# Kernel tuning notes

Hardware: AMD Instinct MI355X
Metric: run time of the kernel (lower is better)

## Reference

```python
import jax, jax.numpy as jnp
import numpy as np

B, S, H, NH = 4, 2048, 768, 12
HD = H // NH

def _ln(x, g, b, eps=1e-5):
    m = jnp.mean(x, -1, keepdims=True)
    v = jnp.mean((x - m) ** 2, -1, keepdims=True)
    return (x - m) * jax.lax.rsqrt(v + eps) * g + b

def setup_inputs() -> dict:
    key = jax.random.key(0)
    ks = jax.random.split(key, 16)
    s = 0.02
    return {
        "x": jax.random.normal(ks[0], (B, S, H), jnp.float32),
        "prev_state": jax.random.normal(ks[1], (B, S, H), jnp.float32),
        "mask": jax.random.randint(ks[2], (B,), 0, 2).astype(bool),
        # depthwise conv1d (groups=H, k=3): torch weight [H, 1, 3] == OIH
        "conv_dw_w": jax.random.normal(ks[3], (H, 1, 3), jnp.float32) * s,
        "conv_dw_b": jnp.zeros((H,), jnp.float32),
        # pointwise conv1d (k=1) stored as [out, in]
        "conv_pw_w": jax.random.normal(ks[4], (H, H), jnp.float32) * s,
        "conv_pw_b": jnp.zeros((H,), jnp.float32),
        "cn_g": jnp.ones((H,), jnp.float32), "cn_b": jnp.zeros((H,), jnp.float32),
        "Wq": jax.random.normal(ks[5], (H, H), jnp.float32) * s, "bq": jnp.zeros((H,), jnp.float32),
        "Wk": jax.random.normal(ks[6], (H, H), jnp.float32) * s, "bk": jnp.zeros((H,), jnp.float32),
        "Wv": jax.random.normal(ks[7], (H, H), jnp.float32) * s, "bv": jnp.zeros((H,), jnp.float32),
        "Wo": jax.random.normal(ks[8], (H, H), jnp.float32) * s, "bo": jnp.zeros((H,), jnp.float32),
        "pn_g": jnp.ones((H,), jnp.float32), "pn_b": jnp.zeros((H,), jnp.float32),
        "Wpost": jax.random.normal(ks[9], (H, H), jnp.float32) * s, "bpost": jnp.zeros((H,), jnp.float32),
        "Wg": jax.random.normal(ks[10], (1, 2 * H), jnp.float32) * s, "bg": jnp.zeros((1,), jnp.float32),
    }

def reference(x, prev_state, mask, conv_dw_w, conv_dw_b, conv_pw_w, conv_pw_b,
              cn_g, cn_b, Wq, bq, Wk, bk, Wv, bv, Wo, bo,
              pn_g, pn_b, Wpost, bpost, Wg, bg):
    # ---- bridge: depthwise conv (k=3) -> pointwise conv (k=1) -> GELU -> LN ----
    mem_t = prev_state.transpose(0, 2, 1)  # [B, H, S]
    dw = jax.lax.conv_general_dilated(
        mem_t, conv_dw_w, window_strides=(1,), padding=[(1, 1)],
        feature_group_count=H, dimension_numbers=("NCH", "OIH", "NCH")) + conv_dw_b[None, :, None]
    pw = jnp.einsum("bhs,oh->bos", dw, conv_pw_w) + conv_pw_b[None, :, None]
    bridged = jax.nn.gelu(pw, approximate=False).transpose(0, 2, 1)  # [B, S, H]
    bridged = _ln(bridged, cn_g, cn_b)
    # ---- cross attention: q from x, k/v from bridged memory (nope, non-causal) ----
    q = (jnp.einsum("bsh,oh->bso", x, Wq) + bq).reshape(B, S, NH, HD)
    k = (jnp.einsum("bsh,oh->bso", bridged, Wk) + bk).reshape(B, S, NH, HD)
    v = (jnp.einsum("bsh,oh->bso", bridged, Wv) + bv).reshape(B, S, NH, HD)
    scores = jnp.einsum("bqnd,bknd->bnqk", q, k) / np.float32(np.sqrt(HD))
    attn = jax.nn.softmax(scores, axis=-1)
    ao = jnp.einsum("bnqk,bknd->bqnd", attn, v).reshape(B, S, H)
    ao = jnp.einsum("bsh,oh->bso", ao, Wo) + bo
    # ---- post-attn norm, linear, gate, scatter-add back under mask ----
    inj = _ln(ao, pn_g, pn_b)
    inj = jnp.einsum("bsh,oh->bso", inj, Wpost) + bpost
    gate = jax.nn.sigmoid(jnp.einsum("bsh,oh->bso", jnp.concatenate([x, bridged], -1), Wg) + bg)
    gated = gate * jnp.tanh(inj)
    mf = mask.astype(x.dtype)[:, None, None]  # batch-row select == masked scatter-add
    out = x + mf * gated
    # masked MSE aux loss (only over selected rows, as in the original)
    denom = jnp.maximum(mask.sum(), 1).astype(x.dtype) * np.float32(S * H)
    aux = jnp.sum(mf * (bridged - x) ** 2) / denom
    return out, aux
```

## Files before the change

kernel.cpp:

```cpp
#include <hip/hip_runtime.h>
#include <math.h>

#define B_ 4
#define S_ 2048
#define H_ 768
#define NH_ 12
#define HD_ 64
#define BSH (B_ * S_ * H_)
#define NROWS (B_ * S_)
#define WSZ (H_ * H_)

typedef __attribute__((ext_vector_type(8))) short bf16x8;
typedef __attribute__((ext_vector_type(4))) short s16x4;
typedef __attribute__((ext_vector_type(4))) float f32x4;
typedef __attribute__((ext_vector_type(2))) unsigned u32x2;
typedef __attribute__((ext_vector_type(4))) unsigned u32x4;

__device__ __forceinline__ short f2bf(float f) {
  union { float f; unsigned u; } x; x.f = f;
  unsigned r = x.u + 0x7FFF + ((x.u >> 16) & 1);
  return (short)(r >> 16);
}
__device__ __forceinline__ float bf2f(short s) {
  union { unsigned u; float f; } x;
  x.u = ((unsigned)(unsigned short)s) << 16;
  return x.f;
}
__device__ __forceinline__ unsigned bfpack(float lo, float hi) {
  union { float f; unsigned u; } a, b; a.f = lo; b.f = hi;
  return __builtin_amdgcn_perm(b.u, a.u, 0x07060302);
}

__device__ __forceinline__ float fexp2(float x) {
#if __has_builtin(__builtin_amdgcn_exp2f)
  return __builtin_amdgcn_exp2f(x);
#else
  float r;
  asm("v_exp_f32 %0, %1" : "=v"(r) : "v"(x));
  return r;
#endif
}

__device__ __forceinline__ void plswap32(unsigned& a, unsigned& b) {
#if __has_builtin(__builtin_amdgcn_permlane32_swap)
  u32x2 r = __builtin_amdgcn_permlane32_swap(a, b, false, false);
  a = r.x; b = r.y;
#else
  asm volatile("v_permlane32_swap_b32 %0, %1" : "+v"(a), "+v"(b));
#endif
}
__device__ __forceinline__ void plswap16(unsigned& a, unsigned& b) {
#if __has_builtin(__builtin_amdgcn_permlane16_swap)
  u32x2 r = __builtin_amdgcn_permlane16_swap(a, b, false, false);
  a = r.x; b = r.y;
#else
  asm volatile("v_permlane16_swap_b32 %0, %1" : "+v"(a), "+v"(b));
#endif
}

typedef __attribute__((address_space(1))) const unsigned int g_u32;
typedef __attribute__((address_space(3))) unsigned int l_u32;
__device__ __forceinline__ void gload16(const void* g, void* l) {
  __builtin_amdgcn_global_load_lds((g_u32*)g, (l_u32*)l, 16, 0, 0);
}

__global__ __launch_bounds__(256) void cvt_x_k(const float* __restrict__ src,
                                               short* __restrict__ dst) {
  int i = (blockIdx.x * 256 + threadIdx.x) * 4;
  float4 v = *(const float4*)(src + i);
  s16x4 o = {f2bf(v.x), f2bf(v.y), f2bf(v.z), f2bf(v.w)};
  *(s16x4*)(dst + i) = o;
}

__global__ __launch_bounds__(256) void cvt6_k(const float* w0, const float* w1,
                                              const float* w2, const float* w3,
                                              const float* w4, const float* w5,
                                              short* __restrict__ dst) {
  int i = (blockIdx.x * 256 + threadIdx.x) * 4;
  int m = i / WSZ;
  int off = i - m * WSZ;
  const float* s = m == 0 ? w0 : m == 1 ? w1 : m == 2 ? w2 : m == 3 ? w3 : m == 4 ? w4 : w5;
  float sc = (m == 1) ? 0.1803368802f : 1.0f;
  float4 v = *(const float4*)(s + off);
  s16x4 o = {f2bf(v.x * sc), f2bf(v.y * sc), f2bf(v.z * sc), f2bf(v.w * sc)};
  *(s16x4*)(dst + i) = o;
}

__global__ __launch_bounds__(192) void dwconv_k(const float* __restrict__ prev,
                                                const float* __restrict__ w3,
                                                const float* __restrict__ bias,
                                                short* __restrict__ out) {
  int row = blockIdx.x;
  int s = row & (S_ - 1);
  int h = threadIdx.x * 4;
  size_t base = (size_t)row * H_ + h;
  float4 c = *(const float4*)(prev + base);
  float4 wa = *(const float4*)(w3 + h * 3);
  float4 wb = *(const float4*)(w3 + h * 3 + 4);
  float4 wc = *(const float4*)(w3 + h * 3 + 8);
  float4 bi = *(const float4*)(bias + h);
  float4 acc;
  acc.x = bi.x + c.x * wa.y;
  acc.y = bi.y + c.y * wb.x;
  acc.z = bi.z + c.z * wb.w;
  acc.w = bi.w + c.w * wc.z;
  if (s > 0) {
    float4 l = *(const float4*)(prev + base - H_);
    acc.x += l.x * wa.x; acc.y += l.y * wa.w; acc.z += l.z * wb.z; acc.w += l.w * wc.y;
  }
  if (s < S_ - 1) {
    float4 r = *(const float4*)(prev + base + H_);
    acc.x += r.x * wa.z; acc.y += r.y * wb.y; acc.z += r.z * wc.x; acc.w += r.w * wc.w;
  }
  s16x4 o = {f2bf(acc.x), f2bf(acc.y), f2bf(acc.z), f2bf(acc.w)};
  *(s16x4*)(out + base) = o;
}

struct GemmJob {
  const short* A; const short* W; const float* bias; short* C; int act; int tout;
  float bscale;
};

__global__ __launch_bounds__(256) void gemm_bf2(GemmJob j0, GemmJob j1, GemmJob j2) {
  int d = blockIdx.x;
  int z = d / 384, r5 = d - z * 384;
  GemmJob j = z == 0 ? j0 : (z == 1 ? j1 : j2);
  int xcd = r5 & 7, s5 = r5 >> 3;
  int nx = s5 % 6, ny = xcd + 8 * (s5 / 6);
  __shared__ short As[128 * 64];
  __shared__ short Ws[128 * 64];
  int tid = threadIdx.x, lane = tid & 63, w = tid >> 6;
  int wr = w >> 1, wc = w & 1, lm = lane & 15, lq = lane >> 4;
  int m0 = ny * 128, n0 = nx * 128;
  int srow = lane >> 3;
  int skc = (lane & 7) * 8;
  const short* gA = j.A + (size_t)(m0 + w * 32 + srow) * H_ + skc;
  const short* gW = j.W + (size_t)(n0 + w * 32 + srow) * H_ + skc;
  short* lA = As + w * 2048;
  short* lW = Ws + w * 2048;

  f32x4 acc[4][4];
#pragma unroll
  for (int i = 0; i < 4; ++i)
#pragma unroll
    for (int jj = 0; jj < 4; ++jj) acc[i][jj] = (f32x4){0.f, 0.f, 0.f, 0.f};

  for (int kt = 0; kt < H_; kt += 64) {
    __syncthreads();
#pragma unroll
    for (int c = 0; c < 4; ++c) {
      gload16(gA + kt + (size_t)(c * 8) * H_, lA + c * 512);
      gload16(gW + kt + (size_t)(c * 8) * H_, lW + c * 512);
    }
    __syncthreads();
#pragma unroll
    for (int kk = 0; kk < 2; ++kk) {
      bf16x8 af[4], wf[4];
#pragma unroll
      for (int i = 0; i < 4; ++i)
        af[i] = *(const bf16x8*)&As[(wr * 64 + i * 16 + lm) * 64 + kk * 32 + lq * 8];
#pragma unroll
      for (int jj = 0; jj < 4; ++jj)
        wf[jj] = *(const bf16x8*)&Ws[(wc * 64 + jj * 16 + lm) * 64 + kk * 32 + lq * 8];
#pragma unroll
      for (int i = 0; i < 4; ++i)
#pragma unroll
        for (int jj = 0; jj < 4; ++jj)
          acc[i][jj] = __builtin_amdgcn_mfma_f32_16x16x32_bf16(af[i], wf[jj], acc[i][jj], 0, 0, 0);
    }
  }

  if (!j.tout) {
#pragma unroll
    for (int jj = 0; jj < 4; ++jj) {
      int col = n0 + wc * 64 + jj * 16 + lm;
      float bn = j.bias[col] * j.bscale;
#pragma unroll
      for (int i = 0; i < 4; ++i) {
        int mrow = m0 + wr * 64 + i * 16 + lq * 4;
#pragma unroll
        for (int r = 0; r < 4; ++r) {
          float cv = acc[i][jj][r] + bn;
          if (j.act) cv = 0.5f * cv * (1.0f + erff(cv * 0.70710678118f));
          j.C[(size_t)(mrow + r) * H_ + col] = f2bf(cv);
        }
      }
    }
  } else {
    int b = m0 >> 11;
    int sb = (m0 & (S_ - 1)) + wr * 64;
#pragma unroll
    for (int jj = 0; jj < 4; ++jj) {
      int col = n0 + wc * 64 + jj * 16 + lm;
      float bn = j.bias[col] * j.bscale;
      short* cp = j.C + ((size_t)(b * H_ + col)) * S_;
#pragma unroll
      for (int i = 0; i < 4; ++i) {
        int s = sb + i * 16 + lq * 4;
        s16x4 pk = {f2bf(acc[i][jj][0] + bn), f2bf(acc[i][jj][1] + bn),
                    f2bf(acc[i][jj][2] + bn), f2bf(acc[i][jj][3] + bn)};
        *(s16x4*)(cp + s) = pk;
      }
    }
  }
}

__global__ __launch_bounds__(256) void gemm_n64(const short* __restrict__ A,
                                                const short* __restrict__ W,
                                                const float* __restrict__ bias,
                                                short* __restrict__ C, int act) {
  int d = blockIdx.x;
  int xcd = d & 7, s5 = d >> 3;
  int nx = s5 % 12, ny = xcd + 8 * (s5 / 12);
  __shared__ short As[128 * 64];
  __shared__ short Ws[64 * 64];
  int tid = threadIdx.x, lane = tid & 63, w = tid >> 6;
  int wm = w >> 1, wn = w & 1, lm = lane & 15, lq = lane >> 4;
  int m0 = ny * 128, n0 = nx * 64;
  const short* gA = A + (size_t)(m0 + w * 32 + (lane >> 3)) * H_ + (lane & 7) * 8;
  const short* gW = W + (size_t)(n0 + w * 16 + (lane >> 3)) * H_ + (lane & 7) * 8;
  short* lA = As + w * 2048;
  short* lW = Ws + w * 1024;

  f32x4 acc[4][2];
#pragma unroll
  for (int i = 0; i < 4; ++i)
#pragma unroll
    for (int jj = 0; jj < 2; ++jj) acc[i][jj] = (f32x4){0.f, 0.f, 0.f, 0.f};

  for (int kt = 0; kt < H_; kt += 64) {
    __syncthreads();
#pragma unroll
    for (int c = 0; c < 4; ++c)
      gload16(gA + kt + (size_t)(c * 8) * H_, lA + c * 512);
#pragma unroll
    for (int c = 0; c < 2; ++c)
      gload16(gW + kt + (size_t)(c * 8) * H_, lW + c * 512);
    __syncthreads();
#pragma unroll
    for (int kk = 0; kk < 2; ++kk) {
      bf16x8 af[4], wf[2];
#pragma unroll
      for (int i = 0; i < 4; ++i)
        af[i] = *(const bf16x8*)&As[(wm * 64 + i * 16 + lm) * 64 + kk * 32 + lq * 8];
#pragma unroll
      for (int jj = 0; jj < 2; ++jj)
        wf[jj] = *(const bf16x8*)&Ws[(wn * 32 + jj * 16 + lm) * 64 + kk * 32 + lq * 8];
#pragma unroll
      for (int i = 0; i < 4; ++i)
#pragma unroll
        for (int jj = 0; jj < 2; ++jj)
          acc[i][jj] = __builtin_amdgcn_mfma_f32_16x16x32_bf16(af[i], wf[jj], acc[i][jj], 0, 0, 0);
    }
  }

#pragma unroll
  for (int jj = 0; jj < 2; ++jj) {
    int col = n0 + wn * 32 + jj * 16 + lm;
    float bn = bias[col];
#pragma unroll
    for (int i = 0; i < 4; ++i) {
      int mrow = m0 + wm * 64 + i * 16 + lq * 4;
#pragma unroll
      for (int r = 0; r < 4; ++r) {
        float cv = acc[i][jj][r] + bn;
        if (act) cv = 0.5f * cv * (1.0f + erff(cv * 0.70710678118f));
        C[(size_t)(mrow + r) * H_ + col] = f2bf(cv);
      }
    }
  }
}

__global__ __launch_bounds__(256) void ln_bf(const short* __restrict__ X,
                                             short* __restrict__ Y,
                                             const float* __restrict__ g,
                                             const float* __restrict__ bb) {
  int row = blockIdx.x;
  size_t base = (size_t)row * H_;
  int h0 = threadIdx.x, h1 = h0 + 256, h2 = h0 + 512;
  float x0 = bf2f(X[base + h0]), x1 = bf2f(X[base + h1]), x2 = bf2f(X[base + h2]);
  float s = x0 + x1 + x2;
  float s2 = x0 * x0 + x1 * x1 + x2 * x2;
  for (int off = 32; off > 0; off >>= 1) {
    s += __shfl_down(s, off);
    s2 += __shfl_down(s2, off);
  }
  __shared__ float sa[4], sq[4], st[2];
  int wid = threadIdx.x >> 6, lane = threadIdx.x & 63;
  if (lane == 0) { sa[wid] = s; sq[wid] = s2; }
  __syncthreads();
  if (threadIdx.x == 0) {
    float ts = sa[0] + sa[1] + sa[2] + sa[3];
    float ts2 = sq[0] + sq[1] + sq[2] + sq[3];
    float mean = ts * (1.0f / H_);
    float var = ts2 * (1.0f / H_) - mean * mean;
    st[0] = mean;
    st[1] = rsqrtf(var + 1e-5f);
  }
  __syncthreads();
  float mean = st[0], rstd = st[1];
  Y[base + h0] = f2bf((x0 - mean) * rstd * g[h0] + bb[h0]);
  Y[base + h1] = f2bf((x1 - mean) * rstd * g[h1] + bb[h1]);
  Y[base + h2] = f2bf((x2 - mean) * rstd * g[h2] + bb[h2]);
}

__global__ __launch_bounds__(256) void attn8_k(const short* __restrict__ qb,
                                               const short* __restrict__ kb,
                                               const short* __restrict__ vtb,
                                               short* __restrict__ aob) {
  __shared__ short Ks[2][64 * 64];
  __shared__ short Vt[2][64 * 64];
  int tid = threadIdx.x, lane = tid & 63, w = tid >> 6;
  int lm = lane & 15, lq = lane >> 4;
  int lm7 = lm & 7;
  int dd = blockIdx.x;
  int xcd = dd & 7, slot = dd >> 3;
  int g = xcd + 8 * (slot >> 4);
  int qx = slot & 15;
  int b = g / NH_, n = g - b * NH_;
  int q0 = qx * 128;
  int hoff = n * HD_;

  int rb8 = (lq ^ lm7) << 3;
  int rb8x = rb8 ^ 32;

  bf16x8 qf[2][2];
#pragma unroll
  for (int qg = 0; qg < 2; ++qg) {
    const short* qrow = qb + ((size_t)(b * S_ + q0 + w * 32 + qg * 16 + lm)) * H_ + hoff;
    qf[qg][0] = *(const bf16x8*)(qrow + lq * 8);
    qf[qg][1] = *(const bf16x8*)(qrow + 32 + lq * 8);
  }

  bf16x8 onef = {0x3F80, 0x3F80, 0x3F80, 0x3F80, 0x3F80, 0x3F80, 0x3F80, 0x3F80};
  f32x4 ls[2];
  ls[0] = (f32x4){0.f, 0.f, 0.f, 0.f};
  ls[1] = (f32x4){0.f, 0.f, 0.f, 0.f};

  f32x4 o[4][2];
#pragma unroll
  for (int i = 0; i < 4; ++i)
#pragma unroll
    for (int qg = 0; qg < 2; ++qg) o[i][qg] = (f32x4){0.f, 0.f, 0.f, 0.f};

  int jl = ((lane & 7) ^ (lane >> 3)) * 8;
  int rr = w * 16 + (lane >> 3);
  const short* kgl = kb + ((size_t)(b * S_ + rr)) * H_ + hoff + jl;
  const short* vgl = vtb + ((size_t)(b * H_ + hoff + rr)) * S_ + jl;
  int lbase = w * 1024;

#pragma unroll
  for (int c = 0; c < 2; ++c) {
    gload16(kgl + (size_t)(c * 8) * H_, &Ks[0][lbase + c * 512]);
    gload16(vgl + (size_t)(c * 8) * S_, &Vt[0][lbase + c * 512]);
  }

  for (int kt = 0, pb = 0; kt < S_; kt += 64, pb ^= 1) {
    __syncthreads();
    if (kt + 64 < S_) {
#pragma unroll
      for (int c = 0; c < 2; ++c) {
        gload16(kgl + (size_t)(kt + 64 + c * 8) * H_, &Ks[pb ^ 1][lbase + c * 512]);
        gload16(vgl + (size_t)(c * 8) * S_ + (kt + 64), &Vt[pb ^ 1][lbase + c * 512]);
      }
    }
    const short* Kw = &Ks[pb][0];
    const short* Vw = &Vt[pb][0];

    f32x4 st[4][2];
    __builtin_amdgcn_s_setprio(1);
#pragma unroll
    for (int ni = 0; ni < 4; ++ni) {
      int krow = (ni * 16 + lm) * 64;
      bf16x8 ka0 = *(const bf16x8*)&Kw[krow + rb8];
      bf16x8 ka1 = *(const bf16x8*)&Kw[krow + rb8x];
#pragma unroll
      for (int qg = 0; qg < 2; ++qg) {
        f32x4 z = (f32x4){0.f, 0.f, 0.f, 0.f};
        z = __builtin_amdgcn_mfma_f32_16x16x32_bf16(ka0, qf[qg][0], z, 0, 0, 0);
        st[ni][qg] = __builtin_amdgcn_mfma_f32_16x16x32_bf16(ka1, qf[qg][1], z, 0, 0, 0);
      }
    }
    __builtin_amdgcn_s_setprio(0);

    bf16x8 pf[2][2];
#pragma unroll
    for (int qg = 0; qg < 2; ++qg) {
      unsigned pw0, pw1, pw2, pw3, pw4, pw5, pw6, pw7;
      {
        float p0 = fexp2(st[0][qg][0]), p1 = fexp2(st[0][qg][1]);
        float p2 = fexp2(st[0][qg][2]), p3 = fexp2(st[0][qg][3]);
        pw0 = bfpack(p0, p1); pw1 = bfpack(p2, p3);
      }
      {
        float p0 = fexp2(st[1][qg][0]), p1 = fexp2(st[1][qg][1]);
        float p2 = fexp2(st[1][qg][2]), p3 = fexp2(st[1][qg][3]);
        pw2 = bfpack(p0, p1); pw3 = bfpack(p2, p3);
      }
      {
        float p0 = fexp2(st[2][qg][0]), p1 = fexp2(st[2][qg][1]);
        float p2 = fexp2(st[2][qg][2]), p3 = fexp2(st[2][qg][3]);
        pw4 = bfpack(p0, p1); pw5 = bfpack(p2, p3);
      }
      {
        float p0 = fexp2(st[3][qg][0]), p1 = fexp2(st[3][qg][1]);
        float p2 = fexp2(st[3][qg][2]), p3 = fexp2(st[3][qg][3]);
        pw6 = bfpack(p0, p1); pw7 = bfpack(p2, p3);
      }
      plswap32(pw0, pw2); plswap16(pw0, pw2);
      plswap32(pw1, pw3); plswap16(pw1, pw3);
      plswap32(pw4, pw6); plswap16(pw4, pw6);
      plswap32(pw5, pw7); plswap16(pw5, pw7);
      union { u32x4 u; bf16x8 v; } c0u, c1u;
      c0u.u = (u32x4){pw0, pw1, pw2, pw3};
      c1u.u = (u32x4){pw4, pw5, pw6, pw7};
      pf[qg][0] = c0u.v;
      pf[qg][1] = c1u.v;
    }

    __builtin_amdgcn_s_setprio(1);
#pragma unroll
    for (int qg = 0; qg < 2; ++qg) {
      ls[qg] = __builtin_amdgcn_mfma_f32_16x16x32_bf16(onef, pf[qg][0], ls[qg], 0, 0, 0);
      ls[qg] = __builtin_amdgcn_mfma_f32_16x16x32_bf16(onef, pf[qg][1], ls[qg], 0, 0, 0);
    }
#pragma unroll
    for (int nd = 0; nd < 4; ++nd) {
      int vrow = (nd * 16 + lm) * 64;
      bf16x8 va0 = *(const bf16x8*)&Vw[vrow + rb8];
      bf16x8 va1 = *(const bf16x8*)&Vw[vrow + rb8x];
#pragma unroll
      for (int qg = 0; qg < 2; ++qg) {
        o[nd][qg] = __builtin_amdgcn_mfma_f32_16x16x32_bf16(va0, pf[qg][0], o[nd][qg], 0, 0, 0);
        o[nd][qg] = __builtin_amdgcn_mfma_f32_16x16x32_bf16(va1, pf[qg][1], o[nd][qg], 0, 0, 0);
      }
    }
    __builtin_amdgcn_s_setprio(0);
  }

#pragma unroll
  for (int qg = 0; qg < 2; ++qg) {
    float inv = 1.0f / ls[qg][0];
    short* orow = aob + ((size_t)(b * S_ + q0 + w * 32 + qg * 16 + lm)) * H_ + hoff;
#pragma unroll
    for (int nd = 0; nd < 4; ++nd) {
      s16x4 pk = {f2bf(o[nd][qg][0] * inv), f2bf(o[nd][qg][1] * inv),
                  f2bf(o[nd][qg][2] * inv), f2bf(o[nd][qg][3] * inv)};
      *(s16x4*)(orow + nd * 16 + lq * 4) = pk;
    }
  }
}

__global__ __launch_bounds__(192) void gate_out_k(const float* __restrict__ x,
                                                  const short* __restrict__ br,
                                                  const short* __restrict__ inj,
                                                  const int* __restrict__ mask,
                                                  const float* __restrict__ Wg,
                                                  const float* __restrict__ bg,
                                                  float* __restrict__ out,
                                                  float* __restrict__ paux) {
  int row = blockIdx.x;
  int b = row >> 11;
  size_t base = (size_t)row * H_;
  int h = threadIdx.x * 4;
  float4 xv = *(const float4*)(x + base + h);
  s16x4 brv = *(const s16x4*)(br + base + h);
  s16x4 inv = *(const s16x4*)(inj + base + h);
  float4 wg0 = *(const float4*)(Wg + h);
  float4 wg1 = *(const float4*)(Wg + H_ + h);
  float b0 = bf2f(brv.x), b1 = bf2f(brv.y), b2 = bf2f(brv.z), b3 = bf2f(brv.w);
  float dot = xv.x * wg0.x + xv.y * wg0.y + xv.z * wg0.z + xv.w * wg0.w
            + b0 * wg1.x + b1 * wg1.y + b2 * wg1.z + b3 * wg1.w;
  float d0 = b0 - xv.x, d1 = b1 - xv.y, d2 = b2 - xv.z, d3 = b3 - xv.w;
  float aux = d0 * d0 + d1 * d1 + d2 * d2 + d3 * d3;
  for (int off = 32; off > 0; off >>= 1) {
    dot += __shfl_down(dot, off);
    aux += __shfl_down(aux, off);
  }
  __shared__ float sd[3], sx[3], gsh[2];
  int wid = threadIdx.x >> 6, lane = threadIdx.x & 63;
  if (lane == 0) { sd[wid] = dot; sx[wid] = aux; }
  __syncthreads();
  if (threadIdx.x == 0) {
    float td = sd[0] + sd[1] + sd[2];
    float ta = sx[0] + sx[1] + sx[2];
    gsh[0] = 1.0f / (1.0f + expf(-(td + bg[0])));
    gsh[1] = ta;
  }
  __syncthreads();
  float mf = (mask[b] != 0) ? 1.0f : 0.0f;
  float gm = gsh[0] * mf;
  float v0 = bf2f(inv.x), v1 = bf2f(inv.y), v2 = bf2f(inv.z), v3 = bf2f(inv.w);
  float e0 = __expf(2.f * v0), e1 = __expf(2.f * v1), e2 = __expf(2.f * v2), e3 = __expf(2.f * v3);
  float4 ov;
  ov.x = xv.x + gm * ((e0 - 1.f) / (e0 + 1.f));
  ov.y = xv.y + gm * ((e1 - 1.f) / (e1 + 1.f));
  ov.z = xv.z + gm * ((e2 - 1.f) / (e2 + 1.f));
  ov.w = xv.w + gm * ((e3 - 1.f) / (e3 + 1.f));
  *(float4*)(out + base + h) = ov;
  if (threadIdx.x == 0) paux[row] = mf * gsh[1];
}

__global__ __launch_bounds__(256) void aux_reduce_k(const float* __restrict__ paux,
                                                    const int* __restrict__ mask,
                                                    float* __restrict__ outp) {
  float s = 0.f;
  for (int i = threadIdx.x; i < NROWS; i += 256) s += paux[i];
  for (int off = 32; off > 0; off >>= 1) s += __shfl_down(s, off);
  __shared__ float sw[4];
  int wid = threadIdx.x >> 6, lane = threadIdx.x & 63;
  if (lane == 0) sw[wid] = s;
  __syncthreads();
  if (threadIdx.x == 0) {
    float t = sw[0] + sw[1] + sw[2] + sw[3];
    int nm = (mask[0] != 0) + (mask[1] != 0) + (mask[2] != 0) + (mask[3] != 0);
    if (nm < 1) nm = 1;
    outp[0] = t / ((float)nm * (float)(S_ * H_));
  }
}

extern "C" void kernel_launch(void* const* d_in, const int* in_sizes, int n_in,
                              void* d_out, int out_size, void* d_ws, size_t ws_size,
                              hipStream_t stream) {
  const float* x     = (const float*)d_in[0];
  const float* prev  = (const float*)d_in[1];
  const int*   mask  = (const int*)d_in[2];
  const float* dw_w  = (const float*)d_in[3];
  const float* dw_b  = (const float*)d_in[4];
  const float* pw_w  = (const float*)d_in[5];
  const float* pw_b  = (const float*)d_in[6];
  const float* cn_g  = (const float*)d_in[7];
  const float* cn_b  = (const float*)d_in[8];
  const float* Wq    = (const float*)d_in[9];
  const float* bq    = (const float*)d_in[10];
  const float* Wk    = (const float*)d_in[11];
  const float* bk    = (const float*)d_in[12];
  const float* Wv    = (const float*)d_in[13];
  const float* bv    = (const float*)d_in[14];
  const float* Wo    = (const float*)d_in[15];
  const float* bo    = (const float*)d_in[16];
  const float* pn_g  = (const float*)d_in[17];
  const float* pn_b  = (const float*)d_in[18];
  const float* Wpost = (const float*)d_in[19];
  const float* bpost = (const float*)d_in[20];
  const float* Wg    = (const float*)d_in[21];
  const float* bg    = (const float*)d_in[22];
  float* out = (float*)d_out;

  short* B0 = (short*)d_ws;
  short* B1 = B0 + BSH;
  short* B2 = B1 + BSH;
  short* B3 = B2 + BSH;
  short* B4 = B3 + BSH;
  short* B5 = B4 + BSH;
  short* WW = B5 + BSH;
  float* paux = (float*)(WW + 6 * WSZ);

  const float C1 = 0.1803368802f;

  GemmJob jq = {B0, WW + WSZ,     bq, B1, 0, 0, C1};
  GemmJob jk = {B3, WW + 2 * WSZ, bk, B4, 0, 0, 1.0f};
  GemmJob jv = {B3, WW + 3 * WSZ, bv, B5, 0, 1, 1.0f};

  cvt6_k<<<6 * WSZ / 1024, 256, 0, stream>>>(pw_w, Wq, Wk, Wv, Wo, Wpost, WW);
  cvt_x_k<<<BSH / 1024, 256, 0, stream>>>(x, B0);
  dwconv_k<<<NROWS, 192, 0, stream>>>(prev, dw_w, dw_b, B1);
  gemm_n64<<<768, 256, 0, stream>>>(B1, WW, pw_b, B2, 1);
  ln_bf<<<NROWS, 256, 0, stream>>>(B2, B3, cn_g, cn_b);
  gemm_bf2<<<1152, 256, 0, stream>>>(jq, jk, jv);
  attn8_k<<<768, 256, 0, stream>>>(B1, B4, B5, B2);
  gemm_n64<<<768, 256, 0, stream>>>(B2, WW + 4 * WSZ, bo, B4, 0);
  ln_bf<<<NROWS, 256, 0, stream>>>(B4, B4, pn_g, pn_b);
  gemm_n64<<<768, 256, 0, stream>>>(B4, WW + 5 * WSZ, bpost, B5, 0);
  gate_out_k<<<NROWS, 192, 0, stream>>>(x, B3, B5, mask, Wg, bg, out, paux);
  aux_reduce_k<<<1, 256, 0, stream>>>(paux, mask, out + BSH);
}
```

Measured before the change: 372.3 us.

## Double-buffer LDS tiles and XOR-swizzle layout in bf16 GEMM kernels

Both GEMM kernels now keep two LDS buffers so the next K-tile's global-to-LDS load is issued before the MFMA work on the current tile. This drops one of the two barriers per iteration. The LDS layout is also XOR-swizzled on 16-byte chunks, with matching swizzled reads, to cut bank conflicts on the fragment loads. In exchange LDS use per block doubles, which may lower occupancy, and correctness depends on gload16 being asynchronous with the single barrier still ordering buffer reuse.

```diff
diff --git a/kernel.cpp b/kernel.cpp
--- a/kernel.cpp
+++ b/kernel.cpp
@@ -127,17 +127,18 @@
   GemmJob j = z == 0 ? j0 : (z == 1 ? j1 : j2);
   int xcd = r5 & 7, s5 = r5 >> 3;
   int nx = s5 % 6, ny = xcd + 8 * (s5 / 6);
-  __shared__ short As[128 * 64];
-  __shared__ short Ws[128 * 64];
+  __shared__ short As[2][128 * 64];
+  __shared__ short Ws[2][128 * 64];
   int tid = threadIdx.x, lane = tid & 63, w = tid >> 6;
   int wr = w >> 1, wc = w & 1, lm = lane & 15, lq = lane >> 4;
+  int lm7 = lm & 7;
+  int rb8 = (lq ^ lm7) << 3, rb8x = rb8 ^ 32;
   int m0 = ny * 128, n0 = nx * 128;
   int srow = lane >> 3;
-  int skc = (lane & 7) * 8;
-  const short* gA = j.A + (size_t)(m0 + w * 32 + srow) * H_ + skc;
-  const short* gW = j.W + (size_t)(n0 + w * 32 + srow) * H_ + skc;
-  short* lA = As + w * 2048;
-  short* lW = Ws + w * 2048;
+  int jl = ((lane & 7) ^ srow) * 8;
+  const short* gA = j.A + (size_t)(m0 + w * 32 + srow) * H_ + jl;
+  const short* gW = j.W + (size_t)(n0 + w * 32 + srow) * H_ + jl;
+  int lbase = w * 2048;
 
   f32x4 acc[4][4];
 #pragma unroll
@@ -145,23 +146,33 @@
 #pragma unroll
     for (int jj = 0; jj < 4; ++jj) acc[i][jj] = (f32x4){0.f, 0.f, 0.f, 0.f};
 
-  for (int kt = 0; kt < H_; kt += 64) {
+#pragma unroll
+  for (int c = 0; c < 4; ++c) {
+    gload16(gA + (size_t)(c * 8) * H_, &As[0][lbase + c * 512]);
+    gload16(gW + (size_t)(c * 8) * H_, &Ws[0][lbase + c * 512]);
+  }
+
+  for (int kt = 0, pb = 0; kt < H_; kt += 64, pb ^= 1) {
     __syncthreads();
-#pragma unroll
-    for (int c = 0; c < 4; ++c) {
-      gload16(gA + kt + (size_t)(c * 8) * H_, lA + c * 512);
-      gload16(gW + kt + (size_t)(c * 8) * H_, lW + c * 512);
-    }
-    __syncthreads();
+    if (kt + 64 < H_) {
+#pragma unroll
+      for (int c = 0; c < 4; ++c) {
+        gload16(gA + kt + 64 + (size_t)(c * 8) * H_, &As[pb ^ 1][lbase + c * 512]);
+        gload16(gW + kt + 64 + (size_t)(c * 8) * H_, &Ws[pb ^ 1][lbase + c * 512]);
+      }
+    }
+    const short* Aw = &As[pb][0];
+    const short* Ww = &Ws[pb][0];
 #pragma unroll
     for (int kk = 0; kk < 2; ++kk) {
+      int ro = kk ? rb8x : rb8;
       bf16x8 af[4], wf[4];
 #pragma unroll
       for (int i = 0; i < 4; ++i)
-        af[i] = *(const bf16x8*)&As[(wr * 64 + i * 16 + lm) * 64 + kk * 32 + lq * 8];
+        af[i] = *(const bf16x8*)&Aw[(wr * 64 + i * 16 + lm) * 64 + ro];
 #pragma unroll
       for (int jj = 0; jj < 4; ++jj)
-        wf[jj] = *(const bf16x8*)&Ws[(wc * 64 + jj * 16 + lm) * 64 + kk * 32 + lq * 8];
+        wf[jj] = *(const bf16x8*)&Ww[(wc * 64 + jj * 16 + lm) * 64 + ro];
 #pragma unroll
       for (int i = 0; i < 4; ++i)
 #pragma unroll
@@ -212,15 +223,19 @@
   int d = blockIdx.x;
   int xcd = d & 7, s5 = d >> 3;
   int nx = s5 % 12, ny = xcd + 8 * (s5 / 12);
-  __shared__ short As[128 * 64];
-  __shared__ short Ws[64 * 64];
+  __shared__ short As[2][128 * 64];
+  __shared__ short Ws[2][64 * 64];
   int tid = threadIdx.x, lane = tid & 63, w = tid >> 6;
   int wm = w >> 1, wn = w & 1, lm = lane & 15, lq = lane >> 4;
+  int lm7 = lm & 7;
+  int rb8 = (lq ^ lm7) << 3, rb8x = rb8 ^ 32;
   int m0 = ny * 128, n0 = nx * 64;
-  const short* gA = A + (size_t)(m0 + w * 32 + (lane >> 3)) * H_ + (lane & 7) * 8;
-  const short* gW = W + (size_t)(n0 + w * 16 + (lane >> 3)) * H_ + (lane & 7) * 8;
-  short* lA = As + w * 2048;
-  short* lW = Ws + w * 1024;
+  int srow = lane >> 3;
+  int jl = ((lane & 7) ^ srow) * 8;
+  const short* gA = A + (size_t)(m0 + w * 32 + srow) * H_ + jl;
+  const short* gW = W + (size_t)(n0 + w * 16 + srow) * H_ + jl;
+  int lbaseA = w * 2048;
+  int lbaseW = w * 1024;
 
   f32x4 acc[4][2];
 #pragma unroll
@@ -228,24 +243,35 @@
 #pragma unroll
     for (int jj = 0; jj < 2; ++jj) acc[i][jj] = (f32x4){0.f, 0.f, 0.f, 0.f};
 
-  for (int kt = 0; kt < H_; kt += 64) {
+#pragma unroll
+  for (int c = 0; c < 4; ++c)
+    gload16(gA + (size_t)(c * 8) * H_, &As[0][lbaseA + c * 512]);
+#pragma unroll
+  for (int c = 0; c < 2; ++c)
+    gload16(gW + (size_t)(c * 8) * H_, &Ws[0][lbaseW + c * 512]);
+
+  for (int kt = 0, pb = 0; kt < H_; kt += 64, pb ^= 1) {
     __syncthreads();
-#pragma unroll
-    for (int c = 0; c < 4; ++c)
-      gload16(gA + kt + (size_t)(c * 8) * H_, lA + c * 512);
-#pragma unroll
-    for (int c = 0; c < 2; ++c)
-      gload16(gW + kt + (size_t)(c * 8) * H_, lW + c * 512);
-    __syncthreads();
+    if (kt + 64 < H_) {
+#pragma unroll
+      for (int c = 0; c < 4; ++c)
+        gload16(gA + kt + 64 + (size_t)(c * 8) * H_, &As[pb ^ 1][lbaseA + c * 512]);
+#pragma unroll
+      for (int c = 0; c < 2; ++c)
+        gload16(gW + kt + 64 + (size_t)(c * 8) * H_, &Ws[pb ^ 1][lbaseW + c * 512]);
+    }
+    const short* Aw = &As[pb][0];
+    const short* Ww = &Ws[pb][0];
 #pragma unroll
     for (int kk = 0; kk < 2; ++kk) {
+      int ro = kk ? rb8x : rb8;
       bf16x8 af[4], wf[2];
 #pragma unroll
       for (int i = 0; i < 4; ++i)
-        af[i] = *(const bf16x8*)&As[(wm * 64 + i * 16 + lm) * 64 + kk * 32 + lq * 8];
+        af[i] = *(const bf16x8*)&Aw[(wm * 64 + i * 16 + lm) * 64 + ro];
 #pragma unroll
       for (int jj = 0; jj < 2; ++jj)
-        wf[jj] = *(const bf16x8*)&Ws[(wn * 32 + jj * 16 + lm) * 64 + kk * 32 + lq * 8];
+        wf[jj] = *(const bf16x8*)&Ww[(wn * 32 + jj * 16 + lm) * 64 + ro];
 #pragma unroll
       for (int i = 0; i < 4; ++i)
 #pragma unroll
```

Result: no change. 369.4 us (-0.8%).
